# Optimization experiments

Hardware: AMD Instinct MI355X
Metric: run time of the kernel (lower is better)

The kernel has to match this reference:

```python
import jax, jax.numpy as jnp
import numpy as np

N_NODES = 20000


def setup_inputs() -> dict:
    key = jax.random.key(0)
    ks = jax.random.split(key, 6)
    d = 512
    E = 640000
    x = jax.random.normal(ks[0], (N_NODES, d), dtype=jnp.float32)
    edge_index = jax.random.randint(ks[1], (2, E), 0, N_NODES, dtype=jnp.int64)
    s = 1.0 / np.sqrt(d)
    W1 = jax.random.uniform(ks[2], (d, d), jnp.float32, -s, s)
    b1 = jax.random.uniform(ks[3], (d,), jnp.float32, -s, s)
    W2 = jax.random.uniform(ks[4], (d, d), jnp.float32, -s, s)
    b2 = jax.random.uniform(ks[5], (d,), jnp.float32, -s, s)
    return {"x": x, "edge_index": edge_index, "W1": W1, "b1": b1, "W2": W2, "b2": b2}


def reference(x, edge_index, W1, b1, W2, b2):
    eps = 0.0
    src, dst = edge_index[0], edge_index[1]
    # scatter-add neighbor aggregation: sum_{j in N(i)} x_j
    agg = jax.ops.segment_sum(x[src], dst, num_segments=N_NODES)  # [N, d]
    h = (1.0 + eps) * x + agg
    # MLP: Linear -> ReLU -> Linear
    h = jax.nn.relu(h @ W1 + b1)
    out = h @ W2 + b2
    return out
```

## Files before the change

### kernel.cpp

```cpp
#include <hip/hip_runtime.h>
#include <hip/hip_bf16.h>

typedef __attribute__((ext_vector_type(8))) short s16x8;
typedef __attribute__((ext_vector_type(4))) float f32x4;

#define D_FEAT 512
#define SLICES 8
#define SLICE_D 64

__device__ __forceinline__ unsigned short f2bf(float f) {
  __hip_bfloat16 h = __float2bfloat16(f);
  return *reinterpret_cast<unsigned short*>(&h);
}

__device__ __forceinline__ float bitsf(unsigned int u) {
  union { unsigned int i; float f; } c;
  c.i = u;
  return c.f;
}

__device__ __forceinline__ void async16(void* lds, const void* g) {
  __builtin_amdgcn_global_load_lds(
      (const __attribute__((address_space(1))) void*)g,
      (__attribute__((address_space(3))) void*)lds, 16, 0, 0);
}


__global__ __launch_bounds__(256) void zero_k(int4* __restrict__ p, int n16) {
  int i = blockIdx.x * 256 + threadIdx.x;
  if (i < n16) p[i] = make_int4(0, 0, 0, 0);
}


__global__ __launch_bounds__(256) void hx_k(const int* __restrict__ dst, int E,
                                            int* __restrict__ deg,
                                            const float* __restrict__ x,
                                            unsigned short* __restrict__ xs, int n8, int hb,
                                            int Nn) {
  int bid = blockIdx.x;
  if (bid < hb) {
    int i = bid * 256 + threadIdx.x;
    if (i < E) atomicAdd(&deg[dst[i]], 1);
  } else {
    int i = (bid - hb) * 256 + threadIdx.x;
    if (i < n8) {
      int n = i >> 6;
      int c = i & 63;
      int s = c >> 3;
      int off = (c & 7);
      const float4* p = (const float4*)x + (size_t)i * 2;
      float4 u = p[0], v = p[1];
      s16x8 r;
      r[0] = (short)f2bf(u.x); r[1] = (short)f2bf(u.y);
      r[2] = (short)f2bf(u.z); r[3] = (short)f2bf(u.w);
      r[4] = (short)f2bf(v.x); r[5] = (short)f2bf(v.y);
      r[6] = (short)f2bf(v.z); r[7] = (short)f2bf(v.w);
      ((s16x8*)xs)[((size_t)s * Nn + n) * 8 + off] = r;
    }
  }
}


__global__ __launch_bounds__(1024) void scan_k(const int* __restrict__ deg,
                                               int* __restrict__ rowstart,
                                               unsigned short* __restrict__ nodeord, int n) {
  __shared__ int wsum[16];
  __shared__ int carry_s;
  __shared__ int hist[65];
  int tid = threadIdx.x;
  int lane = tid & 63, wid = tid >> 6;
  if (tid == 0) carry_s = 0;
  __syncthreads();
  for (int t0 = 0; t0 < n; t0 += 1024) {
    int i = t0 + tid;
    int v = (i < n) ? deg[i] : 0;
    int s = v;
#pragma unroll
    for (int off = 1; off < 64; off <<= 1) {
      int t = __shfl_up(s, off);
      if (lane >= off) s += t;
    }
    if (lane == 63) wsum[wid] = s;
    __syncthreads();
    if (wid == 0) {
      int ws = (lane < 16) ? wsum[lane] : 0;
#pragma unroll
      for (int off = 1; off < 16; off <<= 1) {
        int t = __shfl_up(ws, off);
        if (lane >= off) ws += t;
      }
      if (lane < 16) wsum[lane] = ws;
    }
    __syncthreads();
    int carry = carry_s;
    int wbase = (wid > 0) ? wsum[wid - 1] : 0;
    if (i < n) rowstart[i] = carry + wbase + s - v;
    int total = wsum[15];
    __syncthreads();
    if (tid == 0) carry_s = carry + total;
    __syncthreads();
  }
  if (tid == 0) rowstart[n] = carry_s;
  if (tid < 65) hist[tid] = 0;
  __syncthreads();
  for (int i = tid; i < n; i += 1024) atomicAdd(&hist[min(deg[i], 64)], 1);
  __syncthreads();
  if (tid == 0) {
    int run = 0;
    for (int b = 0; b < 65; ++b) { int c = hist[b]; hist[b] = run; run += c; }
  }
  __syncthreads();
  for (int i = tid; i < n; i += 1024) {
    int b = min(deg[i], 64);
    int pos = atomicAdd(&hist[b], 1);
    nodeord[pos] = (unsigned short)i;
  }
}

__global__ void fill_k(const int* __restrict__ src, const int* __restrict__ dst, int E,
                       const int* __restrict__ rowstart, int* __restrict__ cursor,
                       unsigned short* __restrict__ ep16) {
  int i = blockIdx.x * 256 + threadIdx.x;
  if (i < E) {
    int d = dst[i];
    int pos = atomicAdd(&cursor[d], 1);
    ep16[rowstart[d] + pos] = (unsigned short)src[i];
  }
}


__global__ __launch_bounds__(256, 6) void agg_k(const unsigned short* __restrict__ xs,
                                                const int* __restrict__ rowstart,
                                                const unsigned short* __restrict__ ep16,
                                                const unsigned short* __restrict__ nodeord,
                                                unsigned short* __restrict__ h, int Nn) {
  int slice = blockIdx.x & 7;
  int nb = blockIdx.x >> 3;
  int wid = threadIdx.x >> 6, lane = threadIdx.x & 63;
  int g = lane >> 3, sub = lane & 7;
  int slot = (nb * 4 + wid) * 8 + g;
  int node = nodeord[slot];
  int beg = rowstart[node];
  int deg = rowstart[node + 1] - beg;
  int degm1 = max(deg - 1, 0);
  int dm = deg;
  dm = max(dm, __shfl_xor(dm, 8));
  dm = max(dm, __shfl_xor(dm, 16));
  dm = max(dm, __shfl_xor(dm, 32));
  const s16x8* sb = (const s16x8*)xs + (size_t)slice * Nn * 8;
  s16x8 own = sb[node * 8 + sub];
  float2 acc[4];
#pragma unroll
  for (int q = 0; q < 4; ++q) {
    unsigned int d = (unsigned int)((const int*)&own)[q];
    acc[q].x = bitsf(d << 16);
    acc[q].y = bitsf(d & 0xffff0000u);
  }
  for (int t = 0; t < dm; t += 4) {
    s16x8 v[4];
    float m[4];
#pragma unroll
    for (int b = 0; b < 4; ++b) {
      int tt = t + b;
      int e = ep16[beg + min(tt, degm1)];
      m[b] = (tt < deg) ? 1.f : 0.f;
      v[b] = sb[e * 8 + sub];
    }
#pragma unroll
    for (int b = 0; b < 4; ++b) {
#pragma unroll
      for (int q = 0; q < 4; ++q) {
        unsigned int d = (unsigned int)((const int*)&v[b])[q];
        acc[q].x = fmaf(m[b], bitsf(d << 16), acc[q].x);
        acc[q].y = fmaf(m[b], bitsf(d & 0xffff0000u), acc[q].y);
      }
    }
  }
  s16x8 r;
#pragma unroll
  for (int q = 0; q < 4; ++q) {
    r[q * 2 + 0] = (short)f2bf(acc[q].x);
    r[q * 2 + 1] = (short)f2bf(acc[q].y);
  }
  __builtin_nontemporal_store(r, (s16x8*)(h + (size_t)node * D_FEAT + slice * SLICE_D + sub * 8));
}


__global__ __launch_bounds__(256) void wconv_k(const float* __restrict__ W1,
                                               const float* __restrict__ W2,
                                               unsigned short* __restrict__ W1t,
                                               unsigned short* __restrict__ W2t) {
  __shared__ float tile[64][65];
  int t = blockIdx.x;
  const float* W = W1;
  unsigned short* Wt = W1t;
  if (t >= 64) { t -= 64; W = W2; Wt = W2t; }
  int tr = (t >> 3) * 64;
  int tc = (t & 7) * 64;
  int tid = threadIdx.x;
  int c4 = (tid & 15) * 4, rg = tid >> 4;
#pragma unroll
  for (int rr = 0; rr < 64; rr += 16) {
    int r = rr + rg;
    float4 vv = *(const float4*)&W[(size_t)(tr + r) * 512 + tc + c4];
    tile[r][c4] = vv.x; tile[r][c4 + 1] = vv.y; tile[r][c4 + 2] = vv.z; tile[r][c4 + 3] = vv.w;
  }
  __syncthreads();
  int ch = tid & 15;
#pragma unroll
  for (int rr = 0; rr < 64; rr += 16) {
    int n = rr + rg;
    int k0 = ch * 4;
    ushort4 o;
    o.x = f2bf(tile[k0 + 0][n]);
    o.y = f2bf(tile[k0 + 1][n]);
    o.z = f2bf(tile[k0 + 2][n]);
    o.w = f2bf(tile[k0 + 3][n]);
    *(ushort4*)&Wt[(size_t)(tc + n) * 512 + tr + k0] = o;
  }
}


template <int RELU, int OUTBF16>
__global__ __launch_bounds__(256) void gemm_k(const unsigned short* __restrict__ A,
                                              const unsigned short* __restrict__ Bt,
                                              const float* __restrict__ bias,
                                              void* __restrict__ Cout, int M) {
  const int K = 512;
  const int NSTEP = 16;
  __shared__ unsigned short As[3][128 * 32];
  __shared__ unsigned short Bs[3][128 * 32];
  int mt = (M + 127) >> 7;
  int qx = (mt + 7) >> 3;
  int b = blockIdx.x;
  int x = b & 7, i = b >> 3;
  int tm = x * qx + (i >> 2);
  int tn = i & 3;
  if (tm >= mt) return;
  int tid = threadIdx.x;
  int wave = tid >> 6, lane = tid & 63;
  int lr = lane & 15, lh = lane >> 4;
  int p3 = lr & 3;
  int wm = (wave >> 1) * 64, wn = (wave & 1) * 64;

  auto stage = [&](int pb, int k0) {
#pragma unroll
    for (int ii = 0; ii < 2; ++ii) {
      int cb = ii * 256 + wave * 64 + lane;
      int row = cb >> 2;
      int cg = (cb & 3) ^ (row & 3);
      int ga = tm * 128 + row;
      if (ga > M - 1) ga = M - 1;
      async16(&As[pb][(size_t)(ii * 256 + wave * 64) * 8], A + (size_t)ga * K + k0 + cg * 8);
      int gb = tn * 128 + row;
      async16(&Bs[pb][(size_t)(ii * 256 + wave * 64) * 8], Bt + (size_t)gb * K + k0 + cg * 8);
    }
  };

  f32x4 zero = {0.f, 0.f, 0.f, 0.f};
  f32x4 acc[4][4];
#pragma unroll
  for (int m = 0; m < 4; ++m)
#pragma unroll
    for (int n = 0; n < 4; ++n) acc[m][n] = zero;

  stage(0, 0);
  stage(1, 32);

  for (int t = 0; t < NSTEP; ++t) {
    int pb = t % 3;
    if (t < NSTEP - 1)
      asm volatile("s_waitcnt vmcnt(4)" ::: "memory");
    else
      asm volatile("s_waitcnt vmcnt(0)" ::: "memory");
    __builtin_amdgcn_s_barrier();
    s16x8 av[4], bv[4];
#pragma unroll
    for (int m = 0; m < 4; ++m) {
      int r = wm + m * 16 + lr;
      av[m] = *(const s16x8*)&As[pb][r * 32 + (lh ^ p3) * 8];
    }
#pragma unroll
    for (int n = 0; n < 4; ++n) {
      int r = wn + n * 16 + lr;
      bv[n] = *(const s16x8*)&Bs[pb][r * 32 + (lh ^ p3) * 8];
    }
#pragma unroll
    for (int m = 0; m < 4; ++m)
#pragma unroll
      for (int n = 0; n < 4; ++n)
        acc[m][n] = __builtin_amdgcn_mfma_f32_16x16x32_bf16(av[m], bv[n], acc[m][n], 0, 0, 0);
    __builtin_amdgcn_s_barrier();
    if (t + 2 < NSTEP) stage((t + 2) % 3, (t + 2) * 32);
  }

#pragma unroll
  for (int n = 0; n < 4; ++n) {
    int col = tn * 128 + wn + n * 16 + lr;
    float bval = bias[col];
#pragma unroll
    for (int m = 0; m < 4; ++m) {
#pragma unroll
      for (int j = 0; j < 4; ++j) {
        int row = tm * 128 + wm + m * 16 + lh * 4 + j;
        if (row < M) {
          float v = acc[m][n][j] + bval;
          if (RELU) v = fmaxf(v, 0.f);
          if (OUTBF16)
            ((unsigned short*)Cout)[(size_t)row * 512 + col] = f2bf(v);
          else
            ((float*)Cout)[(size_t)row * 512 + col] = v;
        }
      }
    }
  }
}


extern "C" void kernel_launch(void* const* d_in, const int* in_sizes, int n_in,
                              void* d_out, int out_size, void* d_ws, size_t ws_size,
                              hipStream_t stream) {
  const float* x = (const float*)d_in[0];
  const int* ei = (const int*)d_in[1];
  const float* W1 = (const float*)d_in[2];
  const float* b1 = (const float*)d_in[3];
  const float* W2 = (const float*)d_in[4];
  const float* b2 = (const float*)d_in[5];
  const int N = in_sizes[0] / D_FEAT;
  const int E = in_sizes[1] / 2;
  const int* src = ei;
  const int* dst = ei + E;

  char* w = (char*)d_ws;
  auto alloc = [&](size_t bytes) {
    void* p = (void*)w;
    w += (bytes + 255) & ~(size_t)255;
    return p;
  };
  unsigned short* ep16 = (unsigned short*)alloc((size_t)E * 2 + 256);
  int* deg = (int*)alloc((size_t)N * 4);
  int* cursor = (int*)alloc((size_t)N * 4);
  int* rowstart = (int*)alloc((size_t)(N + 1) * 4);
  unsigned short* nodeord = (unsigned short*)alloc((size_t)N * 2);
  unsigned short* W1t = (unsigned short*)alloc((size_t)512 * 512 * 2);
  unsigned short* W2t = (unsigned short*)alloc((size_t)512 * 512 * 2);
  unsigned short* c1 = (unsigned short*)alloc((size_t)N * 512 * 2);
  unsigned short* h = (unsigned short*)d_out;
  unsigned short* xs = (unsigned short*)d_out + (size_t)N * D_FEAT;

  size_t zbytes = (size_t)((char*)cursor - (char*)deg) + (size_t)N * 4;
  int zn16 = (int)(zbytes / 16);
  zero_k<<<(zn16 + 255) / 256, 256, 0, stream>>>((int4*)deg, zn16);
  int hb = (E + 255) / 256;
  int n8 = N * D_FEAT / 8;
  int xbk = (n8 + 255) / 256;
  hx_k<<<hb + xbk, 256, 0, stream>>>(dst, E, deg, x, xs, n8, hb, N);
  scan_k<<<1, 1024, 0, stream>>>(deg, rowstart, nodeord, N);
  fill_k<<<hb, 256, 0, stream>>>(src, dst, E, rowstart, cursor, ep16);
  wconv_k<<<128, 256, 0, stream>>>(W1, W2, W1t, W2t);
  agg_k<<<8 * (N / 32), 256, 0, stream>>>(xs, rowstart, ep16, nodeord, h, N);
  int mt = (N + 127) / 128, qx = (mt + 7) / 8;
  int grid = 8 * qx * 4;
  gemm_k<1, 1><<<grid, 256, 0, stream>>>(h, W1t, b1, c1, N);
  gemm_k<0, 0><<<grid, 256, 0, stream>>>(c1, W2t, b2, d_out, N);
}
```

Measured before the change: 203.0 us.

## Load GEMM operands directly from global into registers, widen gather unroll to 8

The GEMM drops its LDS triple-buffered async staging and barriers; each wave now loads its A and B fragments straight from global memory into registers, double-buffered across k-steps. The aim is to remove LDS traffic and block-wide synchronisation, relying on L1/L2 to serve the data reuse between waves. The cost is redundant global loads, since waves sharing rows each fetch them, plus possible extra latency exposure. Separately, the neighbor-gather loop now unrolls 8 edges per iteration instead of 4, to keep more loads in flight at the price of more wasted masked loads on low-degree nodes.

```diff
diff --git a/kernel.cpp b/kernel.cpp
--- a/kernel.cpp
+++ b/kernel.cpp
@@ -17,12 +17,6 @@
   union { unsigned int i; float f; } c;
   c.i = u;
   return c.f;
-}
-
-__device__ __forceinline__ void async16(void* lds, const void* g) {
-  __builtin_amdgcn_global_load_lds(
-      (const __attribute__((address_space(1))) void*)g,
-      (__attribute__((address_space(3))) void*)lds, 16, 0, 0);
 }
 
 
@@ -156,18 +150,18 @@
     acc[q].x = bitsf(d << 16);
     acc[q].y = bitsf(d & 0xffff0000u);
   }
-  for (int t = 0; t < dm; t += 4) {
-    s16x8 v[4];
-    float m[4];
-#pragma unroll
-    for (int b = 0; b < 4; ++b) {
+  for (int t = 0; t < dm; t += 8) {
+    s16x8 v[8];
+    float m[8];
+#pragma unroll
+    for (int b = 0; b < 8; ++b) {
       int tt = t + b;
       int e = ep16[beg + min(tt, degm1)];
       m[b] = (tt < deg) ? 1.f : 0.f;
       v[b] = sb[e * 8 + sub];
     }
 #pragma unroll
-    for (int b = 0; b < 4; ++b) {
+    for (int b = 0; b < 8; ++b) {
 #pragma unroll
       for (int q = 0; q < 4; ++q) {
         unsigned int d = (unsigned int)((const int*)&v[b])[q];
@@ -227,9 +221,6 @@
                                               const float* __restrict__ bias,
                                               void* __restrict__ Cout, int M) {
   const int K = 512;
-  const int NSTEP = 16;
-  __shared__ unsigned short As[3][128 * 32];
-  __shared__ unsigned short Bs[3][128 * 32];
   int mt = (M + 127) >> 7;
   int qx = (mt + 7) >> 3;
   int b = blockIdx.x;
@@ -240,22 +231,21 @@
   int tid = threadIdx.x;
   int wave = tid >> 6, lane = tid & 63;
   int lr = lane & 15, lh = lane >> 4;
-  int p3 = lr & 3;
   int wm = (wave >> 1) * 64, wn = (wave & 1) * 64;
 
-  auto stage = [&](int pb, int k0) {
-#pragma unroll
-    for (int ii = 0; ii < 2; ++ii) {
-      int cb = ii * 256 + wave * 64 + lane;
-      int row = cb >> 2;
-      int cg = (cb & 3) ^ (row & 3);
-      int ga = tm * 128 + row;
-      if (ga > M - 1) ga = M - 1;
-      async16(&As[pb][(size_t)(ii * 256 + wave * 64) * 8], A + (size_t)ga * K + k0 + cg * 8);
-      int gb = tn * 128 + row;
-      async16(&Bs[pb][(size_t)(ii * 256 + wave * 64) * 8], Bt + (size_t)gb * K + k0 + cg * 8);
-    }
-  };
+  const unsigned short* arow[4];
+  const unsigned short* brow[4];
+#pragma unroll
+  for (int m = 0; m < 4; ++m) {
+    int r = tm * 128 + wm + m * 16 + lr;
+    if (r > M - 1) r = M - 1;
+    arow[m] = A + (size_t)r * K + lh * 8;
+  }
+#pragma unroll
+  for (int n = 0; n < 4; ++n) {
+    int r = tn * 128 + wn + n * 16 + lr;
+    brow[n] = Bt + (size_t)r * K + lh * 8;
+  }
 
   f32x4 zero = {0.f, 0.f, 0.f, 0.f};
   f32x4 acc[4][4];
@@ -264,35 +254,27 @@
 #pragma unroll
     for (int n = 0; n < 4; ++n) acc[m][n] = zero;
 
-  stage(0, 0);
-  stage(1, 32);
-
-  for (int t = 0; t < NSTEP; ++t) {
-    int pb = t % 3;
-    if (t < NSTEP - 1)
-      asm volatile("s_waitcnt vmcnt(4)" ::: "memory");
-    else
-      asm volatile("s_waitcnt vmcnt(0)" ::: "memory");
-    __builtin_amdgcn_s_barrier();
-    s16x8 av[4], bv[4];
-#pragma unroll
-    for (int m = 0; m < 4; ++m) {
-      int r = wm + m * 16 + lr;
-      av[m] = *(const s16x8*)&As[pb][r * 32 + (lh ^ p3) * 8];
-    }
-#pragma unroll
-    for (int n = 0; n < 4; ++n) {
-      int r = wn + n * 16 + lr;
-      bv[n] = *(const s16x8*)&Bs[pb][r * 32 + (lh ^ p3) * 8];
-    }
-#pragma unroll
-    for (int m = 0; m < 4; ++m)
-#pragma unroll
-      for (int n = 0; n < 4; ++n)
-        acc[m][n] = __builtin_amdgcn_mfma_f32_16x16x32_bf16(av[m], bv[n], acc[m][n], 0, 0, 0);
-    __builtin_amdgcn_s_barrier();
-    if (t + 2 < NSTEP) stage((t + 2) % 3, (t + 2) * 32);
-  }
+  s16x8 avA[4], bvA[4], avB[4], bvB[4];
+#define LOADF(av, bv, t)                                   \
+  _Pragma("unroll") for (int m = 0; m < 4; ++m)            \
+      av[m] = *(const s16x8*)(arow[m] + (t) * 32);         \
+  _Pragma("unroll") for (int n = 0; n < 4; ++n)            \
+      bv[n] = *(const s16x8*)(brow[n] + (t) * 32);
+#define MFMAS(av, bv)                                      \
+  _Pragma("unroll") for (int m = 0; m < 4; ++m)            \
+  _Pragma("unroll") for (int n = 0; n < 4; ++n)            \
+      acc[m][n] = __builtin_amdgcn_mfma_f32_16x16x32_bf16(av[m], bv[n], acc[m][n], 0, 0, 0);
+
+  LOADF(avA, bvA, 0)
+#pragma unroll
+  for (int t = 0; t < 16; t += 2) {
+    if (t + 1 < 16) { LOADF(avB, bvB, t + 1) }
+    MFMAS(avA, bvA)
+    if (t + 2 < 16) { LOADF(avA, bvA, t + 2) }
+    MFMAS(avB, bvB)
+  }
+#undef LOADF
+#undef MFMAS
 
 #pragma unroll
   for (int n = 0; n < 4; ++n) {
```

Result: slower. 255.0 us (+25.6%).

## Fuse weight conversion into scan launch, deepen GEMM pipeline, unroll gather by eight

Applied to the files above, without the earlier changes.

Merges the weight transpose/bf16 conversion kernel into the single-block scan launch, using 128 extra 1024-thread blocks, to remove one launch and overlap the two. The aggregation gather loop issues 8 neighbor loads per iteration instead of 4 to raise memory-level parallelism. The GEMM moves from a 3-stage to a 4-stage async LDS pipeline with adjusted vmcnt waits, which doubles-up prefetch depth but raises LDS use to 64KB per block, possibly lowering occupancy.

```diff
diff --git a/kernel.cpp b/kernel.cpp
--- a/kernel.cpp
+++ b/kernel.cpp
@@ -61,9 +61,36 @@
 }
 
 
-__global__ __launch_bounds__(1024) void scan_k(const int* __restrict__ deg,
-                                               int* __restrict__ rowstart,
-                                               unsigned short* __restrict__ nodeord, int n) {
+__global__ __launch_bounds__(1024) void scanw_k(const int* __restrict__ deg,
+                                                int* __restrict__ rowstart,
+                                                unsigned short* __restrict__ nodeord, int n,
+                                                const float* __restrict__ W1,
+                                                const float* __restrict__ W2,
+                                                unsigned short* __restrict__ W1t,
+                                                unsigned short* __restrict__ W2t) {
+  if (blockIdx.x < 128) {
+    __shared__ float tile[64][65];
+    int t = blockIdx.x;
+    const float* W = W1;
+    unsigned short* Wt = W1t;
+    if (t >= 64) { t -= 64; W = W2; Wt = W2t; }
+    int tr = (t >> 3) * 64;
+    int tc = (t & 7) * 64;
+    int tid = threadIdx.x;
+    int c4 = (tid & 15) * 4, r = tid >> 4;
+    float4 vv = *(const float4*)&W[(size_t)(tr + r) * 512 + tc + c4];
+    tile[r][c4] = vv.x; tile[r][c4 + 1] = vv.y; tile[r][c4 + 2] = vv.z; tile[r][c4 + 3] = vv.w;
+    __syncthreads();
+    int nn = tid >> 4;
+    int k0 = (tid & 15) * 4;
+    ushort4 o;
+    o.x = f2bf(tile[k0 + 0][nn]);
+    o.y = f2bf(tile[k0 + 1][nn]);
+    o.z = f2bf(tile[k0 + 2][nn]);
+    o.w = f2bf(tile[k0 + 3][nn]);
+    *(ushort4*)&Wt[(size_t)(tc + nn) * 512 + tr + k0] = o;
+    return;
+  }
   __shared__ int wsum[16];
   __shared__ int carry_s;
   __shared__ int hist[65];
@@ -156,18 +183,18 @@
     acc[q].x = bitsf(d << 16);
     acc[q].y = bitsf(d & 0xffff0000u);
   }
-  for (int t = 0; t < dm; t += 4) {
-    s16x8 v[4];
-    float m[4];
-#pragma unroll
-    for (int b = 0; b < 4; ++b) {
+  for (int t = 0; t < dm; t += 8) {
+    s16x8 v[8];
+    float m[8];
+#pragma unroll
+    for (int b = 0; b < 8; ++b) {
       int tt = t + b;
       int e = ep16[beg + min(tt, degm1)];
       m[b] = (tt < deg) ? 1.f : 0.f;
       v[b] = sb[e * 8 + sub];
     }
 #pragma unroll
-    for (int b = 0; b < 4; ++b) {
+    for (int b = 0; b < 8; ++b) {
 #pragma unroll
       for (int q = 0; q < 4; ++q) {
         unsigned int d = (unsigned int)((const int*)&v[b])[q];
@@ -183,41 +210,6 @@
     r[q * 2 + 1] = (short)f2bf(acc[q].y);
   }
   __builtin_nontemporal_store(r, (s16x8*)(h + (size_t)node * D_FEAT + slice * SLICE_D + sub * 8));
-}
-
-
-__global__ __launch_bounds__(256) void wconv_k(const float* __restrict__ W1,
-                                               const float* __restrict__ W2,
-                                               unsigned short* __restrict__ W1t,
-                                               unsigned short* __restrict__ W2t) {
-  __shared__ float tile[64][65];
-  int t = blockIdx.x;
-  const float* W = W1;
-  unsigned short* Wt = W1t;
-  if (t >= 64) { t -= 64; W = W2; Wt = W2t; }
-  int tr = (t >> 3) * 64;
-  int tc = (t & 7) * 64;
-  int tid = threadIdx.x;
-  int c4 = (tid & 15) * 4, rg = tid >> 4;
-#pragma unroll
-  for (int rr = 0; rr < 64; rr += 16) {
-    int r = rr + rg;
-    float4 vv = *(const float4*)&W[(size_t)(tr + r) * 512 + tc + c4];
-    tile[r][c4] = vv.x; tile[r][c4 + 1] = vv.y; tile[r][c4 + 2] = vv.z; tile[r][c4 + 3] = vv.w;
-  }
-  __syncthreads();
-  int ch = tid & 15;
-#pragma unroll
-  for (int rr = 0; rr < 64; rr += 16) {
-    int n = rr + rg;
-    int k0 = ch * 4;
-    ushort4 o;
-    o.x = f2bf(tile[k0 + 0][n]);
-    o.y = f2bf(tile[k0 + 1][n]);
-    o.z = f2bf(tile[k0 + 2][n]);
-    o.w = f2bf(tile[k0 + 3][n]);
-    *(ushort4*)&Wt[(size_t)(tc + n) * 512 + tr + k0] = o;
-  }
 }
 
 
@@ -228,8 +220,8 @@
                                               void* __restrict__ Cout, int M) {
   const int K = 512;
   const int NSTEP = 16;
-  __shared__ unsigned short As[3][128 * 32];
-  __shared__ unsigned short Bs[3][128 * 32];
+  __shared__ unsigned short As[4][128 * 32];
+  __shared__ unsigned short Bs[4][128 * 32];
   int mt = (M + 127) >> 7;
   int qx = (mt + 7) >> 3;
   int b = blockIdx.x;
@@ -266,10 +258,14 @@
 
   stage(0, 0);
   stage(1, 32);
-
+  stage(2, 64);
+
+#pragma unroll
   for (int t = 0; t < NSTEP; ++t) {
-    int pb = t % 3;
-    if (t < NSTEP - 1)
+    int pb = t & 3;
+    if (t < NSTEP - 2)
+      asm volatile("s_waitcnt vmcnt(8)" ::: "memory");
+    else if (t == NSTEP - 2)
       asm volatile("s_waitcnt vmcnt(4)" ::: "memory");
     else
       asm volatile("s_waitcnt vmcnt(0)" ::: "memory");
@@ -291,7 +287,7 @@
       for (int n = 0; n < 4; ++n)
         acc[m][n] = __builtin_amdgcn_mfma_f32_16x16x32_bf16(av[m], bv[n], acc[m][n], 0, 0, 0);
     __builtin_amdgcn_s_barrier();
-    if (t + 2 < NSTEP) stage((t + 2) % 3, (t + 2) * 32);
+    if (t + 3 < NSTEP) stage((t + 3) & 3, (t + 3) * 32);
   }
 
 #pragma unroll
@@ -355,9 +351,8 @@
   int n8 = N * D_FEAT / 8;
   int xbk = (n8 + 255) / 256;
   hx_k<<<hb + xbk, 256, 0, stream>>>(dst, E, deg, x, xs, n8, hb, N);
-  scan_k<<<1, 1024, 0, stream>>>(deg, rowstart, nodeord, N);
+  scanw_k<<<129, 1024, 0, stream>>>(deg, rowstart, nodeord, N, W1, W2, W1t, W2t);
   fill_k<<<hb, 256, 0, stream>>>(src, dst, E, rowstart, cursor, ep16);
-  wconv_k<<<128, 256, 0, stream>>>(W1, W2, W1t, W2t);
   agg_k<<<8 * (N / 32), 256, 0, stream>>>(xs, rowstart, ep16, nodeord, h, N);
   int mt = (N + 127) / 128, qx = (mt + 7) / 8;
   int grid = 8 * qx * 4;
```

After: 216.2 us. +6.5%, slower.
